# Optimization experiments

Hardware: AMD Instinct MI355X
Metric: run time of the kernel (lower is better)

Reference implementation:

```python
import jax, jax.numpy as jnp
import numpy as np

B, T, I, H = 64, 512, 128, 2048
SPARSITY = 0.1
SPECTRAL_RADIUS = 0.95


def setup_inputs() -> dict:
    key = jax.random.key(0)
    kx, kin = jax.random.split(key)
    x = jax.random.normal(kx, (B, T, I), dtype=jnp.float32)
    W_in = jax.random.normal(kin, (H, I), dtype=jnp.float32)
    # Build reservoir matrix like the torch module: randn, zeroed where rand < sparsity,
    # then scaled to the target spectral radius.
    rng = np.random.default_rng(0)
    W_res = rng.standard_normal((H, H)).astype(np.float32)
    mask = rng.random((H, H)) < SPARSITY
    W_res = np.where(mask, 0.0, W_res)
    radius = np.max(np.abs(np.linalg.eigvals(W_res))).real
    W_res = (W_res * (SPECTRAL_RADIUS / radius)).astype(np.float32)
    return {"x": x, "W_in": W_in, "W_res": jnp.asarray(W_res)}


def reference(x, W_in, W_res):
    # h_t = tanh(W_in @ x_t^T + W_res @ h_{t-1}^T)^T, expressed batch-major.
    b, t, _ = x.shape
    h0 = jnp.zeros((b, W_res.shape[0]), dtype=x.dtype)

    def step(h, xt):  # h: [B,H], xt: [B,I]
        h_new = jnp.tanh(xt @ W_in.T + h @ W_res.T)
        return h_new, None

    x_tbi = jnp.swapaxes(x, 0, 1)  # [T,B,I]
    h_final, _ = jax.lax.scan(step, h0, x_tbi)
    return h_final  # [B,H]
```

## Files before the change

kernel.cpp:

```cpp
#include <hip/hip_runtime.h>


#define B_ 64
#define T_ 512
#define I_ 128
#define H_ 2048
#define NWG 256
#define ROWS 32
#define BATS 16
#define WPAD 2056
#define IPAD 136
#define PPAD 33
#define FSTRIDE 16

typedef _Float16 f16;
typedef f16 f16x8 __attribute__((ext_vector_type(8)));
typedef float f32x4 __attribute__((ext_vector_type(4)));
typedef unsigned long long u64;
typedef unsigned int u32;
typedef unsigned short u16;
typedef u32 u32x4 __attribute__((ext_vector_type(4)));

#define TAG32 0x00010001u

#define LDS_WRES   0
#define LDS_WINHI  131584
#define LDS_WINLO  (131584 + 8704)
#define LDS_PART   (131584 + 17408)
#define LDS_TOTAL  (131584 + 17408 + 8448)

extern "C" __global__ __launch_bounds__(256, 1)
void esn_kernel(const float* __restrict__ x, const float* __restrict__ Win,
                const float* __restrict__ Wres, float* __restrict__ out,
                u16* ht0, u16* ht1, int* flags)
{
    extern __shared__ char lds[];
    f16*   Wr   = (f16*)(lds + LDS_WRES);
    f16*   Whi  = (f16*)(lds + LDS_WINHI);
    f16*   Wlo  = (f16*)(lds + LDS_WINLO);
    float* part = (float*)(lds + LDS_PART);

    const int tid  = threadIdx.x;
    const int wg   = blockIdx.x;
    const int bg   = (wg & 7) >> 1;
    const int j    = ((wg >> 3) << 1) | (wg & 1);
    const int lid  = (bg << 6) | j;
    const bool leader = (wg < 8);
    const int r0   = j * ROWS;
    const int b0   = bg * BATS;
    const int wv   = tid >> 6;
    const int lane = tid & 63;
    const int lm   = lane & 15;
    const int quad = lane >> 4;

    for (int idx = tid; idx < ROWS * (H_ / 4); idx += 256) {
        int r  = idx >> 9;
        int c4 = idx & 511;
        const float4 v = ((const float4*)(Wres + (size_t)(r0 + r) * H_))[c4];
        f16* dst = Wr + r * WPAD + c4 * 4;
        dst[0] = (f16)v.x; dst[1] = (f16)v.y; dst[2] = (f16)v.z; dst[3] = (f16)v.w;
    }
    for (int idx = tid; idx < ROWS * (I_ / 4); idx += 256) {
        int r  = idx >> 5;
        int c4 = idx & 31;
        const float4 v = ((const float4*)(Win + (size_t)(r0 + r) * I_))[c4];
        float vv[4] = {v.x, v.y, v.z, v.w};
        f16* dh = Whi + r * IPAD + c4 * 4;
        f16* dl = Wlo + r * IPAD + c4 * 4;
        #pragma unroll
        for (int q = 0; q < 4; q++) {
            f16 hi = (f16)vv[q];
            dh[q] = hi;
            dl[q] = (f16)(vv[q] - (float)hi);
        }
    }
    __syncthreads();

    for (int t = 0; t < T_; t++) {
        const u16* hrd = (t & 1) ? ht1 : ht0;
        u16*       hwr = (t & 1) ? ht0 : ht1;
        const u32  E32 = ((t >> 1) & 1) ? TAG32 : 0u;

        f32x4 acc0 = {0.f, 0.f, 0.f, 0.f};
        f32x4 acc1 = {0.f, 0.f, 0.f, 0.f};

        {
            const int kin = wv * 32 + quad * 8;
            const float* xp = x + ((size_t)(b0 + lm) * T_ + t) * I_ + kin;
            float xf[8];
            *(float4*)(xf)     = *(const float4*)(xp);
            *(float4*)(xf + 4) = *(const float4*)(xp + 4);
            f16x8 xhi, xlo;
            #pragma unroll
            for (int qq = 0; qq < 8; qq++) {
                f16 hi = (f16)xf[qq];
                xhi[qq] = hi;
                xlo[qq] = (f16)(xf[qq] - (float)hi);
            }
            f16x8 bh0 = *(const f16x8*)(Whi + lm * IPAD + kin);
            f16x8 bh1 = *(const f16x8*)(Whi + (lm + 16) * IPAD + kin);
            f16x8 bl0 = *(const f16x8*)(Wlo + lm * IPAD + kin);
            f16x8 bl1 = *(const f16x8*)(Wlo + (lm + 16) * IPAD + kin);
            acc0 = __builtin_amdgcn_mfma_f32_16x16x32_f16(xhi, bh0, acc0, 0, 0, 0);
            acc1 = __builtin_amdgcn_mfma_f32_16x16x32_f16(xhi, bh1, acc1, 0, 0, 0);
            acc0 = __builtin_amdgcn_mfma_f32_16x16x32_f16(xlo, bh0, acc0, 0, 0, 0);
            acc1 = __builtin_amdgcn_mfma_f32_16x16x32_f16(xlo, bh1, acc1, 0, 0, 0);
            acc0 = __builtin_amdgcn_mfma_f32_16x16x32_f16(xhi, bl0, acc0, 0, 0, 0);
            acc1 = __builtin_amdgcn_mfma_f32_16x16x32_f16(xhi, bl1, acc1, 0, 0, 0);
        }

        {
            const int* fp = flags + ((t & 1) * NWG + (bg << 6) + (wv << 4)
                                     + (lane & 15)) * FSTRIDE;
            int spins = 0;
            for (;;) {
                int f = __hip_atomic_load(fp, __ATOMIC_RELAXED,
                                          __HIP_MEMORY_SCOPE_AGENT);
                if (__all(f >= t)) break;
                if (++spins > 4096) break;
                __builtin_amdgcn_s_sleep(1);
            }
        }

        if (leader) __builtin_amdgcn_fence(__ATOMIC_ACQUIRE, "agent");

        const u64 hb = (u64)hrd + ((u64)(b0 + lm) << 12) + (wv << 10) + (quad << 4);

        u32x4 v[16];
        #pragma unroll
        for (int ks = 0; ks < 16; ks++) {
            asm volatile("global_load_dwordx4 %0, %1, off sc0"
                         : "=&v"(v[ks]) : "v"(hb + (u64)(ks * 64)));
        }
        asm volatile("s_waitcnt vmcnt(0)" ::: "memory");

        int rounds = 0;
        for (;;) {
            u32 bad = 0;
            #pragma unroll
            for (int ks = 0; ks < 16; ks++) {
                bad |= (v[ks][0] & TAG32) ^ E32;
                bad |= (v[ks][2] & TAG32) ^ E32;
            }
            if (__all(bad == 0)) break;
            ++rounds;
            if (leader) __builtin_amdgcn_fence(__ATOMIC_ACQUIRE, "agent");
            if (bad) {
                __builtin_amdgcn_s_sleep(1);
                if (rounds < 8) {
                    #pragma unroll
                    for (int ks = 0; ks < 16; ks++) {
                        asm volatile("global_load_dwordx4 %0, %1, off sc0"
                                     : "=&v"(v[ks]) : "v"(hb + (u64)(ks * 64)));
                    }
                } else {
                    #pragma unroll
                    for (int ks = 0; ks < 16; ks++) {
                        asm volatile("global_load_dwordx4 %0, %1, off sc0 sc1"
                                     : "=&v"(v[ks]) : "v"(hb + (u64)(ks * 64)));
                    }
                }
            }
            asm volatile("s_waitcnt vmcnt(0)" ::: "memory");
        }

        {
            const f16* w0 = Wr + lm * WPAD + wv * 512 + quad * 8;
            const f16* w1 = Wr + (lm + 16) * WPAD + wv * 512 + quad * 8;
            #pragma unroll
            for (int ks = 0; ks < 16; ks++) {
                f16x8 af;
                #pragma unroll
                for (int e = 0; e < 4; e++)
                    ((u32*)&af)[e] = v[ks][e] & ~TAG32;
                f16x8 bf0 = *(const f16x8*)(w0 + ks * 32);
                f16x8 bf1 = *(const f16x8*)(w1 + ks * 32);
                acc0 = __builtin_amdgcn_mfma_f32_16x16x32_f16(af, bf0, acc0, 0, 0, 0);
                acc1 = __builtin_amdgcn_mfma_f32_16x16x32_f16(af, bf1, acc1, 0, 0, 0);
            }
        }

        {
            float* pw = part + wv * (BATS * PPAD);
            #pragma unroll
            for (int r = 0; r < 4; r++) {
                int m = quad * 4 + r;
                pw[m * PPAD + lm]      = acc0[r];
                pw[m * PPAD + 16 + lm] = acc1[r];
            }
        }
        __syncthreads();

        if (t == T_ - 1) {
            const int m = tid >> 4;
            const int n = (tid & 15) * 2;
            const int o = m * PPAD + n;
            float s0 = part[o]     + part[BATS * PPAD + o]     + part[2 * BATS * PPAD + o]
                     + part[3 * BATS * PPAD + o];
            float s1 = part[o + 1] + part[BATS * PPAD + o + 1] + part[2 * BATS * PPAD + o + 1]
                     + part[3 * BATS * PPAD + o + 1];
            float* op = out + (size_t)(b0 + m) * H_ + r0 + n;
            op[0] = tanhf(s0);
            op[1] = tanhf(s1);
        } else if (tid < 128) {
            const int m  = tid >> 3;
            const int n0 = (tid & 7) * 4;
            const u16 bit = (u16)(((t + 1) >> 1) & 1);
            union { u16 h[4]; u64 u; } pk;
            #pragma unroll
            for (int e = 0; e < 4; e++) {
                const int o = m * PPAD + n0 + e;
                float s = part[o] + part[BATS * PPAD + o] + part[2 * BATS * PPAD + o]
                        + part[3 * BATS * PPAD + o];
                union { f16 f; u16 u; } cv;
                cv.f = (f16)tanhf(s);
                pk.h[e] = (u16)((cv.u & 0xFFFEu) | bit);
            }
            __hip_atomic_store((u64*)(hwr + (size_t)(b0 + m) * H_ + r0 + n0),
                               pk.u, __ATOMIC_RELAXED, __HIP_MEMORY_SCOPE_AGENT);
        }

        __syncthreads();

        if (t < T_ - 1 && tid == 0) {
            __hip_atomic_store(flags + (((t + 1) & 1) * NWG + lid) * FSTRIDE,
                               t + 1, __ATOMIC_RELAXED, __HIP_MEMORY_SCOPE_AGENT);
        }
    }
}

extern "C" void kernel_launch(void* const* d_in, const int* in_sizes, int n_in,
                              void* d_out, int out_size, void* d_ws, size_t ws_size,
                              hipStream_t stream)
{
    (void)in_sizes; (void)n_in; (void)out_size; (void)ws_size;
    const float* x    = (const float*)d_in[0];
    const float* Win  = (const float*)d_in[1];
    const float* Wres = (const float*)d_in[2];
    float* out = (float*)d_out;

    u16* ht0 = (u16*)d_ws;
    u16* ht1 = ht0 + (size_t)B_ * H_;
    int* flags = (int*)((char*)d_ws + (size_t)2 * B_ * H_ * sizeof(u16));

    hipMemsetAsync(d_ws, 0x00, (size_t)B_ * H_ * sizeof(u16), stream);
    hipMemsetAsync((char*)d_ws + (size_t)B_ * H_ * sizeof(u16), 0x01,
                   (size_t)B_ * H_ * sizeof(u16), stream);
    hipMemsetAsync(flags, 0, (size_t)2 * NWG * FSTRIDE * sizeof(int), stream);

    hipFuncSetAttribute((const void*)esn_kernel,
                        hipFuncAttributeMaxDynamicSharedMemorySize, LDS_TOTAL);

    void* args[] = {(void*)&x, (void*)&Win, (void*)&Wres, (void*)&out,
                    (void*)&ht0, (void*)&ht1, (void*)&flags};
    hipLaunchCooperativeKernel((const void*)esn_kernel, dim3(NWG), dim3(256),
                               args, LDS_TOTAL, stream);
}
```

Baseline: 2.477 ms.

## Keep W_res slice in registers, drop flags and LDS reduction, pipeline tagged h loads

Each workgroup now owns 64 hidden rows for 8 batches. Each wave keeps its 16-row slice of W_res as fp16 fragments in registers (64 f16x8 per lane) and covers the full K=2048 itself. That removes the LDS W_res staging, the cross-wave partial-sum reduction, and both __syncthreads per step. The separate flag-array handshake is gone, so readiness rests only on the parity tag bits in the h values. The h loads are split into 8 groups double-buffered across two register sets, so the next group's tag checks and loads overlap the current group's MFMAs. The cost is heavy register pressure, with 256 VGPRs of weights per lane that may spill. Each step also reads 8 rows of h with half-utilized MFMA batch columns, so only lanes with lm < 8 produce output.

```diff
diff --git a/kernel.cpp b/kernel.cpp
--- a/kernel.cpp
+++ b/kernel.cpp
@@ -6,12 +6,9 @@
 #define I_ 128
 #define H_ 2048
 #define NWG 256
-#define ROWS 32
-#define BATS 16
-#define WPAD 2056
+#define ROWS 64
+#define BATS 8
 #define IPAD 136
-#define PPAD 33
-#define FSTRIDE 16
 
 typedef _Float16 f16;
 typedef f16 f16x8 __attribute__((ext_vector_type(8)));
@@ -23,208 +20,165 @@
 
 #define TAG32 0x00010001u
 
-#define LDS_WRES   0
-#define LDS_WINHI  131584
-#define LDS_WINLO  (131584 + 8704)
-#define LDS_PART   (131584 + 17408)
-#define LDS_TOTAL  (131584 + 17408 + 8448)
+#define HLOAD(W, g, BITS) do {                                                 \
+    _Pragma("unroll")                                                          \
+    for (int _i = 0; _i < 8; _i++)                                             \
+        asm volatile("global_load_dwordx4 %0, %1, off " BITS                   \
+                     : "=&v"(W[_i]) : "v"(hb + (u64)(((g) * 8 + _i) * 64)));   \
+} while (0)
+
+#define GPROC(g, W, NWAIT, DO_ISSUE) do {                                      \
+    asm volatile("s_waitcnt vmcnt(" #NWAIT ")" ::: "memory");                  \
+    __builtin_amdgcn_sched_barrier(0);                                         \
+    int rounds_ = 0;                                                           \
+    for (;;) {                                                                 \
+        u32 bad_ = 0;                                                          \
+        _Pragma("unroll")                                                      \
+        for (int _i = 0; _i < 8; _i++) {                                       \
+            bad_ |= (W[_i][0] & TAG32) ^ E32;                \
+            bad_ |= (W[_i][2] & TAG32) ^ E32;                \
+        }                                                                      \
+        if (__all(bad_ == 0)) break;                                           \
+        ++rounds_;                                                             \
+        __builtin_amdgcn_s_sleep(1);                                           \
+        if (rounds_ < 6) {                                                     \
+            HLOAD(W, g, "sc0");                           \
+        } else {                                                               \
+            __builtin_amdgcn_fence(__ATOMIC_ACQUIRE, "agent");                 \
+            HLOAD(W, g, "sc0 sc1");                 \
+        }                                                                      \
+        asm volatile("s_waitcnt vmcnt(0)" ::: "memory");                       \
+        __builtin_amdgcn_sched_barrier(0);                                     \
+    }                                                                          \
+    _Pragma("unroll")                                                          \
+    for (int _i = 0; _i < 8; _i++) {                                           \
+        f16x8 hf_;                                                             \
+        _Pragma("unroll")                                                      \
+        for (int _e = 0; _e < 4; _e++)                                         \
+            ((u32*)&hf_)[_e] = W[_i][_e] & ~TAG32;    \
+        acc[(g) & 3] = __builtin_amdgcn_mfma_f32_16x16x32_f16(                 \
+            bw[(g) * 8 + _i], hf_, acc[(g) & 3], 0, 0, 0);                     \
+    }                                                                          \
+    if (DO_ISSUE) HLOAD(W, (g) + 2, "sc0");                                    \
+} while (0)
 
 extern "C" __global__ __launch_bounds__(256, 1)
 void esn_kernel(const float* __restrict__ x, const float* __restrict__ Win,
                 const float* __restrict__ Wres, float* __restrict__ out,
-                u16* ht0, u16* ht1, int* flags)
+                u16* ht0, u16* ht1)
 {
-    extern __shared__ char lds[];
-    f16*   Wr   = (f16*)(lds + LDS_WRES);
-    f16*   Whi  = (f16*)(lds + LDS_WINHI);
-    f16*   Wlo  = (f16*)(lds + LDS_WINLO);
-    float* part = (float*)(lds + LDS_PART);
+    __shared__ f16 Whi[ROWS][IPAD];
+    __shared__ f16 Wlo[ROWS][IPAD];
 
     const int tid  = threadIdx.x;
     const int wg   = blockIdx.x;
-    const int bg   = (wg & 7) >> 1;
-    const int j    = ((wg >> 3) << 1) | (wg & 1);
-    const int lid  = (bg << 6) | j;
-    const bool leader = (wg < 8);
+    const int bg   = wg & 7;
+    const int j    = wg >> 3;
     const int r0   = j * ROWS;
     const int b0   = bg * BATS;
     const int wv   = tid >> 6;
     const int lane = tid & 63;
     const int lm   = lane & 15;
     const int quad = lane >> 4;
-
-    for (int idx = tid; idx < ROWS * (H_ / 4); idx += 256) {
-        int r  = idx >> 9;
-        int c4 = idx & 511;
-        const float4 v = ((const float4*)(Wres + (size_t)(r0 + r) * H_))[c4];
-        f16* dst = Wr + r * WPAD + c4 * 4;
-        dst[0] = (f16)v.x; dst[1] = (f16)v.y; dst[2] = (f16)v.z; dst[3] = (f16)v.w;
-    }
+    const int lm8  = lm & 7;
+
     for (int idx = tid; idx < ROWS * (I_ / 4); idx += 256) {
         int r  = idx >> 5;
         int c4 = idx & 31;
         const float4 v = ((const float4*)(Win + (size_t)(r0 + r) * I_))[c4];
         float vv[4] = {v.x, v.y, v.z, v.w};
-        f16* dh = Whi + r * IPAD + c4 * 4;
-        f16* dl = Wlo + r * IPAD + c4 * 4;
         #pragma unroll
         for (int q = 0; q < 4; q++) {
             f16 hi = (f16)vv[q];
-            dh[q] = hi;
-            dl[q] = (f16)(vv[q] - (float)hi);
+            Whi[r][c4 * 4 + q] = hi;
+            Wlo[r][c4 * 4 + q] = (f16)(vv[q] - (float)hi);
         }
     }
     __syncthreads();
+
+    f16x8 bw[64];
+    {
+        const float* wp = Wres + (size_t)(r0 + wv * 16 + lm) * H_ + quad * 8;
+        #pragma unroll
+        for (int ks = 0; ks < 64; ks++) {
+            float4 p0 = *(const float4*)(wp + ks * 32);
+            float4 p1 = *(const float4*)(wp + ks * 32 + 4);
+            f16x8 b;
+            b[0] = (f16)p0.x; b[1] = (f16)p0.y; b[2] = (f16)p0.z; b[3] = (f16)p0.w;
+            b[4] = (f16)p1.x; b[5] = (f16)p1.y; b[6] = (f16)p1.z; b[7] = (f16)p1.w;
+            bw[ks] = b;
+        }
+    }
+
+    f32x4 acc[4];
 
     for (int t = 0; t < T_; t++) {
         const u16* hrd = (t & 1) ? ht1 : ht0;
         u16*       hwr = (t & 1) ? ht0 : ht1;
         const u32  E32 = ((t >> 1) & 1) ? TAG32 : 0u;
 
-        f32x4 acc0 = {0.f, 0.f, 0.f, 0.f};
-        f32x4 acc1 = {0.f, 0.f, 0.f, 0.f};
+        #pragma unroll
+        for (int q = 0; q < 4; q++) acc[q] = (f32x4){0.f, 0.f, 0.f, 0.f};
+
+        const u64 hb = (u64)hrd + ((u64)(b0 + lm8) << 12) + (quad << 4);
+
+        u32x4 w0[8], w1[8];
+        HLOAD(w0, 0, "sc0");
+        HLOAD(w1, 1, "sc0");
 
         {
-            const int kin = wv * 32 + quad * 8;
-            const float* xp = x + ((size_t)(b0 + lm) * T_ + t) * I_ + kin;
-            float xf[8];
-            *(float4*)(xf)     = *(const float4*)(xp);
-            *(float4*)(xf + 4) = *(const float4*)(xp + 4);
-            f16x8 xhi, xlo;
+            const float* xp  = x + ((size_t)(b0 + lm8) * T_ + t) * I_ + quad * 8;
+            const f16*   whp = &Whi[wv * 16 + lm][quad * 8];
+            const f16*   wlp = &Wlo[wv * 16 + lm][quad * 8];
             #pragma unroll
-            for (int qq = 0; qq < 8; qq++) {
-                f16 hi = (f16)xf[qq];
-                xhi[qq] = hi;
-                xlo[qq] = (f16)(xf[qq] - (float)hi);
+            for (int k4 = 0; k4 < 4; k4++) {
+                float xf[8];
+                *(float4*)(xf)     = *(const float4*)(xp + k4 * 32);
+                *(float4*)(xf + 4) = *(const float4*)(xp + k4 * 32 + 4);
+                f16x8 xhi, xlo;
+                #pragma unroll
+                for (int q = 0; q < 8; q++) {
+                    f16 hi = (f16)xf[q];
+                    xhi[q] = hi;
+                    xlo[q] = (f16)(xf[q] - (float)hi);
+                }
+                f16x8 wh = *(const f16x8*)(whp + k4 * 32);
+                f16x8 wl = *(const f16x8*)(wlp + k4 * 32);
+                acc[k4] = __builtin_amdgcn_mfma_f32_16x16x32_f16(wh, xhi, acc[k4], 0, 0, 0);
+                acc[k4] = __builtin_amdgcn_mfma_f32_16x16x32_f16(wh, xlo, acc[k4], 0, 0, 0);
+                acc[k4] = __builtin_amdgcn_mfma_f32_16x16x32_f16(wl, xhi, acc[k4], 0, 0, 0);
             }
-            f16x8 bh0 = *(const f16x8*)(Whi + lm * IPAD + kin);
-            f16x8 bh1 = *(const f16x8*)(Whi + (lm + 16) * IPAD + kin);
-            f16x8 bl0 = *(const f16x8*)(Wlo + lm * IPAD + kin);
-            f16x8 bl1 = *(const f16x8*)(Wlo + (lm + 16) * IPAD + kin);
-            acc0 = __builtin_amdgcn_mfma_f32_16x16x32_f16(xhi, bh0, acc0, 0, 0, 0);
-            acc1 = __builtin_amdgcn_mfma_f32_16x16x32_f16(xhi, bh1, acc1, 0, 0, 0);
-            acc0 = __builtin_amdgcn_mfma_f32_16x16x32_f16(xlo, bh0, acc0, 0, 0, 0);
-            acc1 = __builtin_amdgcn_mfma_f32_16x16x32_f16(xlo, bh1, acc1, 0, 0, 0);
-            acc0 = __builtin_amdgcn_mfma_f32_16x16x32_f16(xhi, bl0, acc0, 0, 0, 0);
-            acc1 = __builtin_amdgcn_mfma_f32_16x16x32_f16(xhi, bl1, acc1, 0, 0, 0);
-        }
-
-        {
-            const int* fp = flags + ((t & 1) * NWG + (bg << 6) + (wv << 4)
-                                     + (lane & 15)) * FSTRIDE;
-            int spins = 0;
-            for (;;) {
-                int f = __hip_atomic_load(fp, __ATOMIC_RELAXED,
-                                          __HIP_MEMORY_SCOPE_AGENT);
-                if (__all(f >= t)) break;
-                if (++spins > 4096) break;
-                __builtin_amdgcn_s_sleep(1);
+        }
+
+        GPROC(0, w0, 8, 1);
+        GPROC(1, w1, 8, 1);
+        GPROC(2, w0, 8, 1);
+        GPROC(3, w1, 8, 1);
+        GPROC(4, w0, 8, 1);
+        GPROC(5, w1, 8, 1);
+        GPROC(6, w0, 8, 0);
+        GPROC(7, w1, 0, 0);
+
+        const f32x4 s = (acc[0] + acc[1]) + (acc[2] + acc[3]);
+
+        if (t == T_ - 1) {
+            if (lm < 8) {
+                float4 o;
+                o.x = tanhf(s[0]); o.y = tanhf(s[1]);
+                o.z = tanhf(s[2]); o.w = tanhf(s[3]);
+                *(float4*)(out + (size_t)(b0 + lm) * H_ + r0 + wv * 16 + quad * 4) = o;
             }
-        }
-
-        if (leader) __builtin_amdgcn_fence(__ATOMIC_ACQUIRE, "agent");
-
-        const u64 hb = (u64)hrd + ((u64)(b0 + lm) << 12) + (wv << 10) + (quad << 4);
-
-        u32x4 v[16];
-        #pragma unroll
-        for (int ks = 0; ks < 16; ks++) {
-            asm volatile("global_load_dwordx4 %0, %1, off sc0"
-                         : "=&v"(v[ks]) : "v"(hb + (u64)(ks * 64)));
-        }
-        asm volatile("s_waitcnt vmcnt(0)" ::: "memory");
-
-        int rounds = 0;
-        for (;;) {
-            u32 bad = 0;
-            #pragma unroll
-            for (int ks = 0; ks < 16; ks++) {
-                bad |= (v[ks][0] & TAG32) ^ E32;
-                bad |= (v[ks][2] & TAG32) ^ E32;
-            }
-            if (__all(bad == 0)) break;
-            ++rounds;
-            if (leader) __builtin_amdgcn_fence(__ATOMIC_ACQUIRE, "agent");
-            if (bad) {
-                __builtin_amdgcn_s_sleep(1);
-                if (rounds < 8) {
-                    #pragma unroll
-                    for (int ks = 0; ks < 16; ks++) {
-                        asm volatile("global_load_dwordx4 %0, %1, off sc0"
-                                     : "=&v"(v[ks]) : "v"(hb + (u64)(ks * 64)));
-                    }
-                } else {
-                    #pragma unroll
-                    for (int ks = 0; ks < 16; ks++) {
-                        asm volatile("global_load_dwordx4 %0, %1, off sc0 sc1"
-                                     : "=&v"(v[ks]) : "v"(hb + (u64)(ks * 64)));
-                    }
-                }
-            }
-            asm volatile("s_waitcnt vmcnt(0)" ::: "memory");
-        }
-
-        {
-            const f16* w0 = Wr + lm * WPAD + wv * 512 + quad * 8;
-            const f16* w1 = Wr + (lm + 16) * WPAD + wv * 512 + quad * 8;
-            #pragma unroll
-            for (int ks = 0; ks < 16; ks++) {
-                f16x8 af;
-                #pragma unroll
-                for (int e = 0; e < 4; e++)
-                    ((u32*)&af)[e] = v[ks][e] & ~TAG32;
-                f16x8 bf0 = *(const f16x8*)(w0 + ks * 32);
-                f16x8 bf1 = *(const f16x8*)(w1 + ks * 32);
-                acc0 = __builtin_amdgcn_mfma_f32_16x16x32_f16(af, bf0, acc0, 0, 0, 0);
-                acc1 = __builtin_amdgcn_mfma_f32_16x16x32_f16(af, bf1, acc1, 0, 0, 0);
-            }
-        }
-
-        {
-            float* pw = part + wv * (BATS * PPAD);
-            #pragma unroll
-            for (int r = 0; r < 4; r++) {
-                int m = quad * 4 + r;
-                pw[m * PPAD + lm]      = acc0[r];
-                pw[m * PPAD + 16 + lm] = acc1[r];
-            }
-        }
-        __syncthreads();
-
-        if (t == T_ - 1) {
-            const int m = tid >> 4;
-            const int n = (tid & 15) * 2;
-            const int o = m * PPAD + n;
-            float s0 = part[o]     + part[BATS * PPAD + o]     + part[2 * BATS * PPAD + o]
-                     + part[3 * BATS * PPAD + o];
-            float s1 = part[o + 1] + part[BATS * PPAD + o + 1] + part[2 * BATS * PPAD + o + 1]
-                     + part[3 * BATS * PPAD + o + 1];
-            float* op = out + (size_t)(b0 + m) * H_ + r0 + n;
-            op[0] = tanhf(s0);
-            op[1] = tanhf(s1);
-        } else if (tid < 128) {
-            const int m  = tid >> 3;
-            const int n0 = (tid & 7) * 4;
+        } else if (lm < 8) {
             const u16 bit = (u16)(((t + 1) >> 1) & 1);
             union { u16 h[4]; u64 u; } pk;
             #pragma unroll
             for (int e = 0; e < 4; e++) {
-                const int o = m * PPAD + n0 + e;
-                float s = part[o] + part[BATS * PPAD + o] + part[2 * BATS * PPAD + o]
-                        + part[3 * BATS * PPAD + o];
                 union { f16 f; u16 u; } cv;
-                cv.f = (f16)tanhf(s);
+                cv.f = (f16)tanhf(s[e]);
                 pk.h[e] = (u16)((cv.u & 0xFFFEu) | bit);
             }
-            __hip_atomic_store((u64*)(hwr + (size_t)(b0 + m) * H_ + r0 + n0),
+            __hip_atomic_store((u64*)(hwr + (size_t)(b0 + lm) * H_ + r0 + wv * 16 + quad * 4),
                                pk.u, __ATOMIC_RELAXED, __HIP_MEMORY_SCOPE_AGENT);
-        }
-
-        __syncthreads();
-
-        if (t < T_ - 1 && tid == 0) {
-            __hip_atomic_store(flags + (((t + 1) & 1) * NWG + lid) * FSTRIDE,
-                               t + 1, __ATOMIC_RELAXED, __HIP_MEMORY_SCOPE_AGENT);
         }
     }
 }
@@ -241,18 +195,18 @@
 
     u16* ht0 = (u16*)d_ws;
     u16* ht1 = ht0 + (size_t)B_ * H_;
-    int* flags = (int*)((char*)d_ws + (size_t)2 * B_ * H_ * sizeof(u16));
 
     hipMemsetAsync(d_ws, 0x00, (size_t)B_ * H_ * sizeof(u16), stream);
     hipMemsetAsync((char*)d_ws + (size_t)B_ * H_ * sizeof(u16), 0x01,
                    (size_t)B_ * H_ * sizeof(u16), stream);
-    hipMemsetAsync(flags, 0, (size_t)2 * NWG * FSTRIDE * sizeof(int), stream);
-
-    hipFuncSetAttribute((const void*)esn_kernel,
-                        hipFuncAttributeMaxDynamicSharedMemorySize, LDS_TOTAL);
 
     void* args[] = {(void*)&x, (void*)&Win, (void*)&Wres, (void*)&out,
-                    (void*)&ht0, (void*)&ht1, (void*)&flags};
-    hipLaunchCooperativeKernel((const void*)esn_kernel, dim3(NWG), dim3(256),
-                               args, LDS_TOTAL, stream);
+                    (void*)&ht0, (void*)&ht1};
+    hipError_t ce = hipLaunchCooperativeKernel((const void*)esn_kernel,
+                                               dim3(NWG), dim3(256),
+                                               args, 0, stream);
+    if (ce != hipSuccess) {
+        hipLaunchKernelGGL(esn_kernel, dim3(NWG), dim3(256), 0, stream,
+                           x, Win, Wres, out, ht0, ht1);
+    }
 }
```

After: 8.972 ms. 262% more time.
